# Kernel optimization log

Measured on AMD Instinct MI355X. Metric: run time of the kernel, lower is better.

The kernel has to match this reference:

```python
import jax, jax.numpy as jnp
import numpy as np

B, S, D, H = 2, 2048, 1024, 16
DH = D // H


def setup_inputs() -> dict:
    key = jax.random.key(0)
    ks = jax.random.split(key, 12)
    std = 0.02
    return {
        "q_in": jax.random.normal(ks[0], (B, S, D), jnp.float32),
        "k_in": jax.random.normal(ks[1], (B, S, D), jnp.float32),
        "v_in": jax.random.normal(ks[2], (B, S, D), jnp.float32),
        "mask": jnp.zeros((B, 1, S, S), jnp.float32),
        "Wq": jax.random.truncated_normal(ks[3], -2., 2., (D, D), jnp.float32) * std,
        "bq": jnp.zeros((D,), jnp.float32),
        "Wk": jax.random.truncated_normal(ks[4], -2., 2., (D, D), jnp.float32) * std,
        "bk": jnp.zeros((D,), jnp.float32),
        "Wv": jax.random.truncated_normal(ks[5], -2., 2., (D, D), jnp.float32) * std,
        "bv": jnp.zeros((D,), jnp.float32),
        "Wo": jax.random.truncated_normal(ks[6], -2., 2., (D, D), jnp.float32) * std,
        "bo": jnp.zeros((D,), jnp.float32),
    }


def reference(q_in, k_in, v_in, mask, Wq, bq, Wk, bk, Wv, bv, Wo, bo):
    # projections: [B,S,D]
    q = q_in @ Wq + bq
    k = k_in @ Wk + bk
    v = v_in @ Wv + bv
    # split heads -> [B,H,S,DH]
    def split(x):
        return x.reshape(B, -1, H, DH).transpose(0, 2, 1, 3)
    q, k, v = split(q), split(k), split(v)
    # scaled dot-product attention (dropout is identity: training=False)
    scale = 1.0 / jnp.sqrt(jnp.float32(DH))
    scores = jnp.einsum("bhqd,bhkd->bhqk", q, k) * scale + mask
    attn = jax.nn.softmax(scores, axis=-1)
    ctx = jnp.einsum("bhqk,bhkd->bhqd", attn, v)
    # merge heads -> [B,S,D]
    ctx = ctx.transpose(0, 2, 1, 3).reshape(B, -1, D)
    out = ctx @ Wo + bo
    return out, attn
```

## Files before the change

### kernel.cpp

```cpp
#include <hip/hip_runtime.h>

#define B_  2
#define S_  2048
#define D_  1024
#define H_  16
#define DH_ 64

typedef _Float16 f16x8 __attribute__((ext_vector_type(8)));
typedef float    f32x4 __attribute__((ext_vector_type(4)));

#define MFMA16(a, b, c) __builtin_amdgcn_mfma_f32_16x16x32_f16((a), (b), (c), 0, 0, 0)

#define GLD16(gptr, lptr)                                                           \
    __builtin_amdgcn_global_load_lds(                                               \
        (const __attribute__((address_space(1))) void*)(gptr),                      \
        (__attribute__((address_space(3))) void*)(lptr), 16, 0, 0)

__global__ __launch_bounds__(256) void cvt_x(
    const float* __restrict__ q, const float* __restrict__ k, const float* __restrict__ v,
    _Float16* __restrict__ x16)
{
    const int z = blockIdx.y;
    const float* src = (z == 0) ? q : (z == 1) ? k : v;
    _Float16* dst = x16 + (size_t)z * (4096 * 1024);
    const size_t i = ((size_t)blockIdx.x * 256 + threadIdx.x) * 8;
    float4 a = *(const float4*)(src + i);
    float4 b = *(const float4*)(src + i + 4);
    f16x8 o = { (_Float16)a.x, (_Float16)a.y, (_Float16)a.z, (_Float16)a.w,
                (_Float16)b.x, (_Float16)b.y, (_Float16)b.z, (_Float16)b.w };
    *(f16x8*)(dst + i) = o;
}

__global__ __launch_bounds__(256) void cvt_w(
    const float* __restrict__ Wq, const float* __restrict__ Wk,
    const float* __restrict__ Wv, const float* __restrict__ Wo,
    _Float16* __restrict__ Wt3,
    _Float16* __restrict__ Wot)
{
    const int z = blockIdx.z;
    const float* W = (z == 0) ? Wq : (z == 1) ? Wk : (z == 2) ? Wv : Wo;
    _Float16* Wt = (z < 3) ? (Wt3 + (size_t)z * (1024 * 1024)) : Wot;

    __shared__ _Float16 T[64][72];
    const int k0 = blockIdx.y * 64, n0 = blockIdx.x * 64;
    const int r = threadIdx.x >> 3, c8 = (threadIdx.x & 7) * 8;

#pragma unroll
    for (int it = 0; it < 2; ++it) {
        const int row = it * 32 + r;
        const float* p = W + (size_t)(k0 + row) * D_ + n0 + c8;
        float4 a = *(const float4*)p;
        float4 b = *(const float4*)(p + 4);
        _Float16* t = &T[row][c8];
        t[0] = (_Float16)a.x; t[1] = (_Float16)a.y; t[2] = (_Float16)a.z; t[3] = (_Float16)a.w;
        t[4] = (_Float16)b.x; t[5] = (_Float16)b.y; t[6] = (_Float16)b.z; t[7] = (_Float16)b.w;
    }
    __syncthreads();
#pragma unroll
    for (int it = 0; it < 2; ++it) {
        const int nrow = it * 32 + r;
        f16x8 o = { T[c8 + 0][nrow], T[c8 + 1][nrow], T[c8 + 2][nrow], T[c8 + 3][nrow],
                    T[c8 + 4][nrow], T[c8 + 5][nrow], T[c8 + 6][nrow], T[c8 + 7][nrow] };
        *(f16x8*)(Wt + (size_t)(n0 + nrow) * D_ + k0 + c8) = o;
    }
}

__global__ __launch_bounds__(256) void gemm_qkv_f(
    const _Float16* __restrict__ X16, const _Float16* __restrict__ Wt3,
    const float* __restrict__ bq, const float* __restrict__ bk, const float* __restrict__ bv,
    _Float16* __restrict__ QKVh)
{
    const int z = blockIdx.z;
    const _Float16* Ag = X16 + (size_t)z * (4096 * 1024);
    const _Float16* Bg = Wt3 + (size_t)z * (1024 * 1024);
    const float* bias = (z == 0) ? bq : (z == 1) ? bk : bv;
    _Float16* dst = QKVh + (size_t)z * (4096 * 1024);

    __shared__ _Float16 As[128 * 32];
    __shared__ _Float16 Bs[128 * 32];

    const int tid = threadIdx.x, lane = tid & 63, wave = tid >> 6;
    const int quad = lane >> 4, col = lane & 15;
    const int wm = wave >> 1, wn = wave & 1;
    const int bm0 = blockIdx.y * 128, bn0 = blockIdx.x * 128;

    const int srow = lane >> 2;
    const int ska  = (lane & 3) * 8;

    f32x4 acc[4][4] = {};

    for (int k0 = 0; k0 < D_; k0 += 32) {
#pragma unroll
        for (int i = 0; i < 2; ++i) {
            const int ch = wave * 2 + i;
            const int row = ch * 16 + srow;
            GLD16(Ag + (size_t)(bm0 + row) * D_ + k0 + ska, &As[ch * 512]);
            GLD16(Bg + (size_t)(bn0 + row) * D_ + k0 + ska, &Bs[ch * 512]);
        }
        __syncthreads();

        f16x8 a[4], b[4];
#pragma unroll
        for (int r = 0; r < 4; ++r)
            a[r] = *(const f16x8*)&As[(wm * 64 + r * 16 + col) * 32 + quad * 8];
#pragma unroll
        for (int c = 0; c < 4; ++c)
            b[c] = *(const f16x8*)&Bs[(wn * 64 + c * 16 + col) * 32 + quad * 8];
#pragma unroll
        for (int r = 0; r < 4; ++r)
#pragma unroll
            for (int c = 0; c < 4; ++c)
                acc[r][c] = MFMA16(a[r], b[c], acc[r][c]);
        __syncthreads();
    }

#pragma unroll
    for (int r = 0; r < 4; ++r)
#pragma unroll
        for (int c = 0; c < 4; ++c) {
            const int n = bn0 + wn * 64 + c * 16 + col;
            const int h = n >> 6, dh = n & 63;
            const float bi = bias[n];
#pragma unroll
            for (int e = 0; e < 4; ++e) {
                const int m = bm0 + wm * 64 + r * 16 + quad * 4 + e;
                const int bb = m >> 11, s = m & 2047;
                dst[(((size_t)(bb * H_ + h)) * S_ + s) * DH_ + dh] =
                    (_Float16)(acc[r][c][e] + bi);
            }
        }
}

__global__ __launch_bounds__(256) void gemm_out_f(
    const _Float16* __restrict__ Ag, const _Float16* __restrict__ Bg,
    const float* __restrict__ bias, float* __restrict__ out)
{
    __shared__ _Float16 As[128 * 32];
    __shared__ _Float16 Bs[128 * 32];

    const int tid = threadIdx.x, lane = tid & 63, wave = tid >> 6;
    const int quad = lane >> 4, col = lane & 15;
    const int wm = wave >> 1, wn = wave & 1;
    const int bm0 = blockIdx.y * 128, bn0 = blockIdx.x * 128;

    const int srow = lane >> 2;
    const int ska  = (lane & 3) * 8;

    f32x4 acc[4][4] = {};

    for (int k0 = 0; k0 < D_; k0 += 32) {
#pragma unroll
        for (int i = 0; i < 2; ++i) {
            const int ch = wave * 2 + i;
            const int row = ch * 16 + srow;
            GLD16(Ag + (size_t)(bm0 + row) * D_ + k0 + ska, &As[ch * 512]);
            GLD16(Bg + (size_t)(bn0 + row) * D_ + k0 + ska, &Bs[ch * 512]);
        }
        __syncthreads();

        f16x8 a[4], b[4];
#pragma unroll
        for (int r = 0; r < 4; ++r)
            a[r] = *(const f16x8*)&As[(wm * 64 + r * 16 + col) * 32 + quad * 8];
#pragma unroll
        for (int c = 0; c < 4; ++c)
            b[c] = *(const f16x8*)&Bs[(wn * 64 + c * 16 + col) * 32 + quad * 8];
#pragma unroll
        for (int r = 0; r < 4; ++r)
#pragma unroll
            for (int c = 0; c < 4; ++c)
                acc[r][c] = MFMA16(a[r], b[c], acc[r][c]);
        __syncthreads();
    }

#pragma unroll
    for (int r = 0; r < 4; ++r)
#pragma unroll
        for (int c = 0; c < 4; ++c) {
            const int n = bn0 + wn * 64 + c * 16 + col;
            const float bi = bias[n];
#pragma unroll
            for (int e = 0; e < 4; ++e) {
                const int m = bm0 + wm * 64 + r * 16 + quad * 4 + e;
                out[(size_t)m * D_ + n] = acc[r][c][e] + bi;
            }
        }
}

__global__ __launch_bounds__(256) void attn_kernel(
    const _Float16* __restrict__ Qh, const _Float16* __restrict__ Kh,
    const _Float16* __restrict__ Vh, const float* __restrict__ mask,
    float* __restrict__ attn, _Float16* __restrict__ ctx)
{
    const int bh = blockIdx.y;
    const int b = bh >> 4, h = bh & 15;
    const int qb0 = blockIdx.x * 64;
    const int tid = threadIdx.x, lane = tid & 63, wave = tid >> 6;
    const int quad = lane >> 4, col = lane & 15;

    __shared__ _Float16 Ks[32][72];
    __shared__ _Float16 Vts[64][40];
    __shared__ _Float16 Ps[4][16][40];

    const int qrow0 = qb0 + wave * 16;

    const _Float16* qp = Qh + ((size_t)bh * S_ + qrow0 + col) * DH_;
    const f16x8 aq0 = *(const f16x8*)(qp + quad * 8);
    const f16x8 aq1 = *(const f16x8*)(qp + 32 + quad * 8);

    const float LOG2E = 1.4426950408889634f;
    const float scale_l2 = 0.125f * LOG2E;

    float mrow[4] = { -1e30f, -1e30f, -1e30f, -1e30f };
    float lrow[4] = { 0.f, 0.f, 0.f, 0.f };

    const int krow = tid >> 3, kc8 = (tid & 7) * 8;

    for (int kt = 0; kt < S_; kt += 32) {
        *(f16x8*)&Ks[krow][kc8] =
            *(const f16x8*)(Kh + ((size_t)bh * S_ + kt + krow) * DH_ + kc8);
        __syncthreads();
#pragma unroll
        for (int c = 0; c < 2; ++c) {
            f16x8 b0 = *(const f16x8*)&Ks[c * 16 + col][quad * 8];
            f16x8 b1 = *(const f16x8*)&Ks[c * 16 + col][32 + quad * 8];
            f32x4 sc = {};
            sc = MFMA16(aq0, b0, sc);
            sc = MFMA16(aq1, b1, sc);
#pragma unroll
            for (int e = 0; e < 4; ++e) {
                const int q = qrow0 + quad * 4 + e;
                const float s2 = sc[e] * scale_l2 +
                    mask[((size_t)b * S_ + q) * S_ + kt + c * 16 + col] * LOG2E;
                const float nm = fmaxf(mrow[e], s2);
                lrow[e] = lrow[e] * exp2f(mrow[e] - nm) + exp2f(s2 - nm);
                mrow[e] = nm;
            }
        }
        __syncthreads();
    }

#pragma unroll
    for (int off = 1; off < 16; off <<= 1) {
#pragma unroll
        for (int e = 0; e < 4; ++e) {
            const float om = __shfl_xor(mrow[e], off, 64);
            const float ol = __shfl_xor(lrow[e], off, 64);
            const float nm = fmaxf(mrow[e], om);
            lrow[e] = lrow[e] * exp2f(mrow[e] - nm) + ol * exp2f(om - nm);
            mrow[e] = nm;
        }
    }
    float invl[4];
#pragma unroll
    for (int e = 0; e < 4; ++e) invl[e] = 1.0f / lrow[e];

    f32x4 cacc[4] = {};
    for (int kt = 0; kt < S_; kt += 32) {
        *(f16x8*)&Ks[krow][kc8] =
            *(const f16x8*)(Kh + ((size_t)bh * S_ + kt + krow) * DH_ + kc8);
        {
            f16x8 v0 = *(const f16x8*)(Vh + ((size_t)bh * S_ + kt + krow) * DH_ + kc8);
#pragma unroll
            for (int j = 0; j < 8; ++j) Vts[kc8 + j][krow] = v0[j];
        }
        __syncthreads();

#pragma unroll
        for (int c = 0; c < 2; ++c) {
            f16x8 b0 = *(const f16x8*)&Ks[c * 16 + col][quad * 8];
            f16x8 b1 = *(const f16x8*)&Ks[c * 16 + col][32 + quad * 8];
            f32x4 sc = {};
            sc = MFMA16(aq0, b0, sc);
            sc = MFMA16(aq1, b1, sc);
#pragma unroll
            for (int e = 0; e < 4; ++e) {
                const int q = qrow0 + quad * 4 + e;
                const float s2 = sc[e] * scale_l2 +
                    mask[((size_t)b * S_ + q) * S_ + kt + c * 16 + col] * LOG2E;
                const float p = exp2f(s2 - mrow[e]) * invl[e];
                attn[((size_t)bh * S_ + q) * S_ + kt + c * 16 + col] = p;
                Ps[wave][quad * 4 + e][c * 16 + col] = (_Float16)p;
            }
        }

        {
            f16x8 apf = *(const f16x8*)&Ps[wave][col][quad * 8];
#pragma unroll
            for (int nt = 0; nt < 4; ++nt) {
                f16x8 bv = *(const f16x8*)&Vts[nt * 16 + col][quad * 8];
                cacc[nt] = MFMA16(apf, bv, cacc[nt]);
            }
        }
        __syncthreads();
    }

#pragma unroll
    for (int nt = 0; nt < 4; ++nt)
#pragma unroll
        for (int e = 0; e < 4; ++e) {
            const int s = qrow0 + quad * 4 + e;
            const int d = h * DH_ + nt * 16 + col;
            ctx[((size_t)b * S_ + s) * D_ + d] = (_Float16)cacc[nt][e];
        }
}

extern "C" void kernel_launch(void* const* d_in, const int* in_sizes, int n_in,
                              void* d_out, int out_size, void* d_ws, size_t ws_size,
                              hipStream_t stream) {
    const float* q_in = (const float*)d_in[0];
    const float* k_in = (const float*)d_in[1];
    const float* v_in = (const float*)d_in[2];
    const float* mask = (const float*)d_in[3];
    const float* Wq   = (const float*)d_in[4];
    const float* bq   = (const float*)d_in[5];
    const float* Wk   = (const float*)d_in[6];
    const float* bk   = (const float*)d_in[7];
    const float* Wv   = (const float*)d_in[8];
    const float* bv   = (const float*)d_in[9];
    const float* Wo   = (const float*)d_in[10];
    const float* bo   = (const float*)d_in[11];

    float* out  = (float*)d_out;
    float* attn = out + (size_t)B_ * S_ * D_;

    const size_t elems = (size_t)B_ * H_ * S_ * DH_;

    _Float16* Qh  = (_Float16*)d_ws;
    _Float16* Kh  = Qh + elems;
    _Float16* Vh  = Kh + elems;
    _Float16* Ctx = Vh + elems;
    _Float16* Wot = Ctx + elems;

    _Float16* X16 = (_Float16*)attn;
    _Float16* Wt3 = X16 + 3 * elems;

    cvt_x<<<dim3(2048, 3), 256, 0, stream>>>(q_in, k_in, v_in, X16);
    cvt_w<<<dim3(16, 16, 4), 256, 0, stream>>>(Wq, Wk, Wv, Wo, Wt3, Wot);
    gemm_qkv_f<<<dim3(8, 32, 3), 256, 0, stream>>>(X16, Wt3, bq, bk, bv, Qh);
    attn_kernel<<<dim3(32, 32), 256, 0, stream>>>(Qh, Kh, Vh, mask, attn, Ctx);
    gemm_out_f<<<dim3(8, 32), 256, 0, stream>>>(Ctx, Wot, bo, out);
}
```

Before: 930.1 us.

## Store V transposed and K swizzled, stage attention tiles via global_load_lds

```diff
diff --git a/kernel.cpp b/kernel.cpp
--- a/kernel.cpp
+++ b/kernel.cpp
@@ -7,6 +7,7 @@
 #define DH_ 64
 
 typedef _Float16 f16x8 __attribute__((ext_vector_type(8)));
+typedef _Float16 f16x4 __attribute__((ext_vector_type(4)));
 typedef float    f32x4 __attribute__((ext_vector_type(4)));
 
 #define MFMA16(a, b, c) __builtin_amdgcn_mfma_f32_16x16x32_f16((a), (b), (c), 0, 0, 0)
@@ -34,8 +35,7 @@
 __global__ __launch_bounds__(256) void cvt_w(
     const float* __restrict__ Wq, const float* __restrict__ Wk,
     const float* __restrict__ Wv, const float* __restrict__ Wo,
-    _Float16* __restrict__ Wt3,
-    _Float16* __restrict__ Wot)
+    _Float16* __restrict__ Wt3, _Float16* __restrict__ Wot)
 {
     const int z = blockIdx.z;
     const float* W = (z == 0) ? Wq : (z == 1) ? Wk : (z == 2) ? Wv : Wo;
@@ -114,21 +114,54 @@
         __syncthreads();
     }
 
-#pragma unroll
-    for (int r = 0; r < 4; ++r)
-#pragma unroll
-        for (int c = 0; c < 4; ++c) {
-            const int n = bn0 + wn * 64 + c * 16 + col;
-            const int h = n >> 6, dh = n & 63;
-            const float bi = bias[n];
-#pragma unroll
-            for (int e = 0; e < 4; ++e) {
-                const int m = bm0 + wm * 64 + r * 16 + quad * 4 + e;
-                const int bb = m >> 11, s = m & 2047;
-                dst[(((size_t)(bb * H_ + h)) * S_ + s) * DH_ + dh] =
-                    (_Float16)(acc[r][c][e] + bi);
-            }
-        }
+    if (z == 2) {
+#pragma unroll
+        for (int r = 0; r < 4; ++r)
+#pragma unroll
+            for (int c = 0; c < 4; ++c) {
+                const int n = bn0 + wn * 64 + c * 16 + col;
+                const int h = n >> 6, dh = n & 63;
+                const float bi = bias[n];
+                const int m0 = bm0 + wm * 64 + r * 16 + quad * 4;
+                const int bb = m0 >> 11, s0 = m0 & 2047;
+                f16x4 pk = { (_Float16)(acc[r][c][0] + bi), (_Float16)(acc[r][c][1] + bi),
+                             (_Float16)(acc[r][c][2] + bi), (_Float16)(acc[r][c][3] + bi) };
+                const int kin = (s0 & ~63) + ((s0 & 63) ^ ((dh & 7) * 8));
+                *(f16x4*)(dst + ((size_t)(bb * H_ + h) * DH_ + dh) * S_ + kin) = pk;
+            }
+    } else if (z == 1) {
+#pragma unroll
+        for (int r = 0; r < 4; ++r)
+#pragma unroll
+            for (int c = 0; c < 4; ++c) {
+                const int n = bn0 + wn * 64 + c * 16 + col;
+                const int h = n >> 6, dh = n & 63;
+                const float bi = bias[n];
+#pragma unroll
+                for (int e = 0; e < 4; ++e) {
+                    const int m = bm0 + wm * 64 + r * 16 + quad * 4 + e;
+                    const int bb = m >> 11, s = m & 2047;
+                    dst[(((size_t)(bb * H_ + h)) * S_ + s) * DH_ + (dh ^ ((s & 7) * 8))] =
+                        (_Float16)(acc[r][c][e] + bi);
+                }
+            }
+    } else {
+#pragma unroll
+        for (int r = 0; r < 4; ++r)
+#pragma unroll
+            for (int c = 0; c < 4; ++c) {
+                const int n = bn0 + wn * 64 + c * 16 + col;
+                const int h = n >> 6, dh = n & 63;
+                const float bi = bias[n];
+#pragma unroll
+                for (int e = 0; e < 4; ++e) {
+                    const int m = bm0 + wm * 64 + r * 16 + quad * 4 + e;
+                    const int bb = m >> 11, s = m & 2047;
+                    dst[(((size_t)(bb * H_ + h)) * S_ + s) * DH_ + dh] =
+                        (_Float16)(acc[r][c][e] + bi);
+                }
+            }
+    }
 }
 
 __global__ __launch_bounds__(256) void gemm_out_f(
@@ -189,7 +222,7 @@
 
 __global__ __launch_bounds__(256) void attn_kernel(
     const _Float16* __restrict__ Qh, const _Float16* __restrict__ Kh,
-    const _Float16* __restrict__ Vh, const float* __restrict__ mask,
+    const _Float16* __restrict__ Vt, const float* __restrict__ mask,
     float* __restrict__ attn, _Float16* __restrict__ ctx)
 {
     const int bh = blockIdx.y;
@@ -198,9 +231,9 @@
     const int tid = threadIdx.x, lane = tid & 63, wave = tid >> 6;
     const int quad = lane >> 4, col = lane & 15;
 
-    __shared__ _Float16 Ks[32][72];
-    __shared__ _Float16 Vts[64][40];
-    __shared__ _Float16 Ps[4][16][40];
+    __shared__ __align__(16) _Float16 Ks[64 * 64];
+    __shared__ __align__(16) _Float16 Vs[64 * 64];
+    __shared__ __align__(16) _Float16 Ps[4][16][72];
 
     const int qrow0 = qb0 + wave * 16;
 
@@ -214,28 +247,42 @@
     float mrow[4] = { -1e30f, -1e30f, -1e30f, -1e30f };
     float lrow[4] = { 0.f, 0.f, 0.f, 0.f };
 
-    const int krow = tid >> 3, kc8 = (tid & 7) * 8;
-
-    for (int kt = 0; kt < S_; kt += 32) {
-        *(f16x8*)&Ks[krow][kc8] =
-            *(const f16x8*)(Kh + ((size_t)bh * S_ + kt + krow) * DH_ + kc8);
-        __syncthreads();
-#pragma unroll
-        for (int c = 0; c < 2; ++c) {
-            f16x8 b0 = *(const f16x8*)&Ks[c * 16 + col][quad * 8];
-            f16x8 b1 = *(const f16x8*)&Ks[c * 16 + col][32 + quad * 8];
+    const int srow = lane >> 3;
+    const int sb   = (lane & 7) * 8;
+
+    for (int kt = 0; kt < S_; kt += 64) {
+#pragma unroll
+        for (int r = 0; r < 2; ++r) {
+            const int row0 = r * 32 + wave * 8;
+            GLD16(Kh + ((size_t)bh * S_ + kt + row0 + srow) * DH_ + sb, &Ks[row0 * DH_]);
+        }
+        __syncthreads();
+
+        float s2a[4][4];
+#pragma unroll
+        for (int c = 0; c < 4; ++c) {
+            const int rk = c * 16 + col;
+            const int kx = (quad * 8) ^ ((rk & 7) * 8);
+            f16x8 b0 = *(const f16x8*)&Ks[rk * 64 + kx];
+            f16x8 b1 = *(const f16x8*)&Ks[rk * 64 + (kx ^ 32)];
             f32x4 sc = {};
             sc = MFMA16(aq0, b0, sc);
             sc = MFMA16(aq1, b1, sc);
 #pragma unroll
             for (int e = 0; e < 4; ++e) {
                 const int q = qrow0 + quad * 4 + e;
-                const float s2 = sc[e] * scale_l2 +
-                    mask[((size_t)b * S_ + q) * S_ + kt + c * 16 + col] * LOG2E;
-                const float nm = fmaxf(mrow[e], s2);
-                lrow[e] = lrow[e] * exp2f(mrow[e] - nm) + exp2f(s2 - nm);
-                mrow[e] = nm;
-            }
+                s2a[c][e] = sc[e] * scale_l2 +
+                    mask[((size_t)b * S_ + q) * S_ + kt + rk] * LOG2E;
+            }
+        }
+#pragma unroll
+        for (int e = 0; e < 4; ++e) {
+            float nm = fmaxf(fmaxf(mrow[e], s2a[0][e]), fmaxf(s2a[1][e], s2a[2][e]));
+            nm = fmaxf(nm, s2a[3][e]);
+            lrow[e] = lrow[e] * exp2f(mrow[e] - nm)
+                    + exp2f(s2a[0][e] - nm) + exp2f(s2a[1][e] - nm)
+                    + exp2f(s2a[2][e] - nm) + exp2f(s2a[3][e] - nm);
+            mrow[e] = nm;
         }
         __syncthreads();
     }
@@ -251,45 +298,48 @@
             mrow[e] = nm;
         }
     }
-    float invl[4];
-#pragma unroll
-    for (int e = 0; e < 4; ++e) invl[e] = 1.0f / lrow[e];
+    float moff[4];
+#pragma unroll
+    for (int e = 0; e < 4; ++e) moff[e] = mrow[e] + log2f(lrow[e]);
 
     f32x4 cacc[4] = {};
-    for (int kt = 0; kt < S_; kt += 32) {
-        *(f16x8*)&Ks[krow][kc8] =
-            *(const f16x8*)(Kh + ((size_t)bh * S_ + kt + krow) * DH_ + kc8);
-        {
-            f16x8 v0 = *(const f16x8*)(Vh + ((size_t)bh * S_ + kt + krow) * DH_ + kc8);
-#pragma unroll
-            for (int j = 0; j < 8; ++j) Vts[kc8 + j][krow] = v0[j];
-        }
-        __syncthreads();
-
-#pragma unroll
-        for (int c = 0; c < 2; ++c) {
-            f16x8 b0 = *(const f16x8*)&Ks[c * 16 + col][quad * 8];
-            f16x8 b1 = *(const f16x8*)&Ks[c * 16 + col][32 + quad * 8];
+    for (int kt = 0; kt < S_; kt += 64) {
+#pragma unroll
+        for (int r = 0; r < 2; ++r) {
+            const int row0 = r * 32 + wave * 8;
+            GLD16(Kh + ((size_t)bh * S_ + kt + row0 + srow) * DH_ + sb, &Ks[row0 * DH_]);
+            GLD16(Vt + ((size_t)bh * DH_ + row0 + srow) * S_ + kt + sb, &Vs[row0 * DH_]);
+        }
+        __syncthreads();
+
+#pragma unroll
+        for (int c = 0; c < 4; ++c) {
+            const int rk = c * 16 + col;
+            const int kx = (quad * 8) ^ ((rk & 7) * 8);
+            f16x8 b0 = *(const f16x8*)&Ks[rk * 64 + kx];
+            f16x8 b1 = *(const f16x8*)&Ks[rk * 64 + (kx ^ 32)];
             f32x4 sc = {};
             sc = MFMA16(aq0, b0, sc);
             sc = MFMA16(aq1, b1, sc);
 #pragma unroll
             for (int e = 0; e < 4; ++e) {
                 const int q = qrow0 + quad * 4 + e;
-                const float s2 = sc[e] * scale_l2 +
-                    mask[((size_t)b * S_ + q) * S_ + kt + c * 16 + col] * LOG2E;
-                const float p = exp2f(s2 - mrow[e]) * invl[e];
-                attn[((size_t)bh * S_ + q) * S_ + kt + c * 16 + col] = p;
-                Ps[wave][quad * 4 + e][c * 16 + col] = (_Float16)p;
-            }
-        }
-
-        {
-            f16x8 apf = *(const f16x8*)&Ps[wave][col][quad * 8];
+                const float p = exp2f(sc[e] * scale_l2 +
+                    mask[((size_t)b * S_ + q) * S_ + kt + rk] * LOG2E - moff[e]);
+                attn[((size_t)bh * S_ + q) * S_ + kt + rk] = p;
+                Ps[wave][quad * 4 + e][rk] = (_Float16)p;
+            }
+        }
+
+#pragma unroll
+        for (int ks = 0; ks < 2; ++ks) {
+            f16x8 ap = *(const f16x8*)&Ps[wave][col][ks * 32 + quad * 8];
 #pragma unroll
             for (int nt = 0; nt < 4; ++nt) {
-                f16x8 bv = *(const f16x8*)&Vts[nt * 16 + col][quad * 8];
-                cacc[nt] = MFMA16(apf, bv, cacc[nt]);
+                const int rd = nt * 16 + col;
+                const int vx = (ks * 32 + quad * 8) ^ ((rd & 7) * 8);
+                f16x8 bv = *(const f16x8*)&Vs[rd * 64 + vx];
+                cacc[nt] = MFMA16(ap, bv, cacc[nt]);
             }
         }
         __syncthreads();
```

New measurement: 1.003 ms. 7.8% more time.
